# Kernel optimization log

Measured on AMD Instinct MI355X. Metric: run time of the kernel, lower is better.

## Reference

```python
import jax, jax.numpy as jnp
import numpy as np

# Tree: 64 leaves (16 feat -> 16 out), 8 mids (16 feat + 8*16 child = 144 -> 32 out),
# root (16 feat + 8*32 child = 272 -> 64 out), head -> 10 tasks. Eval-mode BatchNorm.
B = 16384
EPS = 1e-5


def setup_inputs() -> dict:
    key = jax.random.key(0)
    ks = jax.random.split(key, 24)
    rn = lambda k, s: jax.random.normal(k, s, dtype=jnp.float32)
    ru = lambda k, s: jax.random.uniform(k, s, dtype=jnp.float32)
    return {
        "x": rn(ks[0], (B, 1168)),
        # leaf layers (64 nodes, 16 -> 16)
        "Wl": rn(ks[1], (64, 16, 16)) * 0.1, "bl": rn(ks[2], (64, 16)) * 0.1,
        "gl": ru(ks[3], (64, 16)) + 0.5, "betal": rn(ks[4], (64, 16)) * 0.1,
        "ml": rn(ks[5], (64, 16)) * 0.1, "vl": ru(ks[6], (64, 16)) + 0.5,
        # mid layers (8 nodes, 144 -> 32)
        "Wm": rn(ks[7], (8, 144, 32)) * 0.1, "bm": rn(ks[8], (8, 32)) * 0.1,
        "gm": ru(ks[9], (8, 32)) + 0.5, "betam": rn(ks[10], (8, 32)) * 0.1,
        "mm": rn(ks[11], (8, 32)) * 0.1, "vm": ru(ks[12], (8, 32)) + 0.5,
        # root layer (272 -> 64)
        "Wr": rn(ks[13], (272, 64)) * 0.1, "br": rn(ks[14], (64,)) * 0.1,
        "gr": ru(ks[15], (64,)) + 0.5, "betar": rn(ks[16], (64,)) * 0.1,
        "mr": rn(ks[17], (64,)) * 0.1, "vr": ru(ks[18], (64,)) + 0.5,
        # root prediction head (64 -> 10 tasks)
        "Wh": rn(ks[19], (64, 10)) * 0.1, "bh": rn(ks[20], (10,)) * 0.1,
    }


def _bn(h, g, b, m, v):
    return (h - m) * jax.lax.rsqrt(v + EPS) * g + b


def reference(x, Wl, bl, gl, betal, ml, vl, Wm, bm, gm, betam, mm, vm,
              Wr, br, gr, betar, mr, vr, Wh, bh):
    n = x.shape[0]
    # leaves: gather own features (contiguous layout), Linear+BN+Tanh, batched over 64 nodes
    xl = x[:, :1024].reshape(n, 64, 16)
    hl = jnp.tanh(_bn(jnp.einsum('bli,lio->blo', xl, Wl) + bl, gl, betal, ml, vl))
    # mids: concat own features with 8 leaf-child outputs -> [n, 8, 144]
    xm = x[:, 1024:1152].reshape(n, 8, 16)
    mid_in = jnp.concatenate([xm, hl.reshape(n, 8, 128)], axis=-1)
    hm = jnp.tanh(_bn(jnp.einsum('bmi,mio->bmo', mid_in, Wm) + bm, gm, betam, mm, vm))
    # root: concat own features with 8 mid outputs -> [n, 272]
    root_in = jnp.concatenate([x[:, 1152:1168], hm.reshape(n, 256)], axis=-1)
    hr = jnp.tanh(_bn(root_in @ Wr + br, gr, betar, mr, vr))
    # root prediction head (eval-mode forward returns only root prediction)
    return hr @ Wh + bh
```

## Files before the change

kernel.cpp:

```cpp
#include <hip/hip_runtime.h>

typedef __attribute__((ext_vector_type(8))) short bf16x8;
typedef __attribute__((ext_vector_type(4))) float f32x4;

#define EPS 1e-5f

#define N_FRAG_BLOCKS 182
#define WSB_LEAF 0
#define WSB_MID  64
#define WSB_ROOT 144
#define WSB_HEAD 180
#define ST_SL 0
#define ST_TL 1024
#define ST_SM 2048
#define ST_TM 2304
#define ST_SR 2560
#define ST_TR 2624
#define WS_ST_BYTE_OFF (N_FRAG_BLOCKS * 1024)

__device__ __forceinline__ unsigned short f2bf(float f) {
    unsigned u = __float_as_uint(f);
    unsigned r = u + 0x7fffu + ((u >> 16) & 1u);
    return (unsigned short)(r >> 16);
}

__device__ __forceinline__ unsigned pack2bf(float a, float b) {
    return (unsigned)f2bf(a) | ((unsigned)f2bf(b) << 16);
}

__device__ __forceinline__ bf16x8 pack8(float4 a, float4 b) {
    union { unsigned u[4]; bf16x8 v; } r;
    r.u[0] = pack2bf(a.x, a.y); r.u[1] = pack2bf(a.z, a.w);
    r.u[2] = pack2bf(b.x, b.y); r.u[3] = pack2bf(b.z, b.w);
    return r.v;
}

__device__ __forceinline__ float tanh_fast(float x) {
    float e = __expf(2.0f * x);
    return 1.0f - 2.0f / (e + 1.0f);
}

__global__ void ontology_prep(
    const float* __restrict__ Wl, const float* __restrict__ Wm,
    const float* __restrict__ Wr, const float* __restrict__ Wh,
    const float* __restrict__ bl, const float* __restrict__ gl,
    const float* __restrict__ betal, const float* __restrict__ ml,
    const float* __restrict__ vl,
    const float* __restrict__ bm, const float* __restrict__ gm,
    const float* __restrict__ betam, const float* __restrict__ mm,
    const float* __restrict__ vm,
    const float* __restrict__ br, const float* __restrict__ gr,
    const float* __restrict__ betar, const float* __restrict__ mr,
    const float* __restrict__ vr,
    unsigned short* __restrict__ wsFrag, float* __restrict__ wsST)
{
    const int b = blockIdx.x;
    const int t = threadIdx.x;
    if (b < N_FRAG_BLOCKS) {
        const int row = t & 15, g = t >> 4;
        unsigned short vals[8];
        #pragma unroll
        for (int i = 0; i < 8; ++i) {
            const int k = g * 8 + i;
            float v = 0.f;
            if (b < 64) {
                const int l = b;
                if ((l & 1) == 0) { if (k < 16)  v = Wl[l * 256 + k * 16 + row]; }
                else              { if (k >= 16) v = Wl[l * 256 + (k - 16) * 16 + row]; }
            } else if (b < 144) {
                const int idx = b - 64, m = idx / 10, rem = idx % 10;
                const int tt = rem / 5, s = rem % 5;
                const int krow = s * 32 + k;
                if (krow < 144) v = Wm[m * 4608 + krow * 32 + tt * 16 + row];
            } else if (b < 180) {
                const int idx = b - 144, tt = idx / 9, s = idx % 9;
                if (s == 0) { if (k < 16) v = Wr[k * 64 + tt * 16 + row]; }
                else { const int krow = 16 + (s - 1) * 32 + k;
                       v = Wr[krow * 64 + tt * 16 + row]; }
            } else {
                const int s = b - 180, krow = s * 32 + k;
                if (row < 10) v = Wh[krow * 10 + row];
            }
            vals[i] = f2bf(v);
        }
        #pragma unroll
        for (int i = 0; i < 8; ++i) wsFrag[b * 512 + t * 8 + i] = vals[i];
    } else if (b == N_FRAG_BLOCKS) {
        for (int i = 0; i < 16; ++i) {
            const int id = t + 64 * i;
            const float S = gl[id] * rsqrtf(vl[id] + EPS);
            wsST[ST_SL + id] = S;
            wsST[ST_TL + id] = (bl[id] - ml[id]) * S + betal[id];
        }
    } else if (b == N_FRAG_BLOCKS + 1) {
        for (int i = 0; i < 4; ++i) {
            const int id = t + 64 * i;
            const float S = gm[id] * rsqrtf(vm[id] + EPS);
            wsST[ST_SM + id] = S;
            wsST[ST_TM + id] = (bm[id] - mm[id]) * S + betam[id];
        }
    } else {
        const int id = t;
        const float S = gr[id] * rsqrtf(vr[id] + EPS);
        wsST[ST_SR + id] = S;
        wsST[ST_TR + id] = (br[id] - mr[id]) * S + betar[id];
    }
}

__global__ __launch_bounds__(256, 4) void ontology_mfma(
    const float* __restrict__ x,
    const unsigned short* __restrict__ wsFrag,
    const float* __restrict__ wsST,
    const float* __restrict__ bh,
    float* __restrict__ out)
{
    __shared__ __align__(16) unsigned short mid_in[4][16][168];
    __shared__ __align__(16) unsigned short hm[16][264];
    unsigned short (*hr)[72] = (unsigned short (*)[72])&mid_in[0][0][0];

    const int w    = threadIdx.x >> 6;
    const int lane = threadIdx.x & 63;
    const int c    = lane & 15;
    const int g    = lane >> 4;
    const int rowbase = blockIdx.x * 16;
    const float* xrow = x + (size_t)(rowbase + c) * 1168;

    {
        uint2 z = {0u, 0u};
        *(uint2*)&mid_in[w][c][144 + 4 * g] = z;
    }

    const float* Sl = wsST + ST_SL, *Tl = wsST + ST_TL;
    const float* Sm = wsST + ST_SM, *Tm = wsST + ST_TM;
    const float* Sr = wsST + ST_SR, *Tr = wsST + ST_TR;

    #pragma unroll 1
    for (int mi = 0; mi < 2; ++mi) {
        const int mm = w * 2 + mi;
        {
            float4 xm4 = *(const float4*)(xrow + 1024 + mm * 16 + 4 * g);
            uint2 p; p.x = pack2bf(xm4.x, xm4.y); p.y = pack2bf(xm4.z, xm4.w);
            *(uint2*)&mid_in[w][c][4 * g] = p;
        }
        #pragma unroll
        for (int p = 0; p < 4; ++p) {
            const int pair = mm * 4 + p;
            const float* xp = xrow + pair * 32 + g * 8;
            float4 xa = *(const float4*)xp;
            float4 xb = *(const float4*)(xp + 4);
            bf16x8 bfrag = pack8(xa, xb);
            #pragma unroll
            for (int e = 0; e < 2; ++e) {
                const int leaf = pair * 2 + e;
                bf16x8 afrag = *(const bf16x8*)(wsFrag + (WSB_LEAF + leaf) * 512 + lane * 8);
                f32x4 acc = {0.f, 0.f, 0.f, 0.f};
                acc = __builtin_amdgcn_mfma_f32_16x16x32_bf16(afrag, bfrag, acc, 0, 0, 0);
                float4 S = *(const float4*)(Sl + leaf * 16 + 4 * g);
                float4 T = *(const float4*)(Tl + leaf * 16 + 4 * g);
                float h0 = tanh_fast(acc[0] * S.x + T.x);
                float h1 = tanh_fast(acc[1] * S.y + T.y);
                float h2 = tanh_fast(acc[2] * S.z + T.z);
                float h3 = tanh_fast(acc[3] * S.w + T.w);
                uint2 pk; pk.x = pack2bf(h0, h1); pk.y = pack2bf(h2, h3);
                *(uint2*)&mid_in[w][c][16 + (p * 2 + e) * 16 + 4 * g] = pk;
            }
        }
        {
            f32x4 acc0 = {0.f, 0.f, 0.f, 0.f};
            f32x4 acc1 = {0.f, 0.f, 0.f, 0.f};
            const unsigned short* fb = wsFrag + (WSB_MID + mm * 10) * 512 + lane * 8;
            #pragma unroll
            for (int s = 0; s < 5; ++s) {
                bf16x8 bfrag = *(const bf16x8*)&mid_in[w][c][s * 32 + g * 8];
                bf16x8 a0 = *(const bf16x8*)(fb + s * 512);
                bf16x8 a1 = *(const bf16x8*)(fb + (5 + s) * 512);
                acc0 = __builtin_amdgcn_mfma_f32_16x16x32_bf16(a0, bfrag, acc0, 0, 0, 0);
                acc1 = __builtin_amdgcn_mfma_f32_16x16x32_bf16(a1, bfrag, acc1, 0, 0, 0);
            }
            #pragma unroll
            for (int t = 0; t < 2; ++t) {
                f32x4 acc = t ? acc1 : acc0;
                const int po = mm * 32 + t * 16 + 4 * g;
                float4 S = *(const float4*)(Sm + po);
                float4 T = *(const float4*)(Tm + po);
                float h0 = tanh_fast(acc[0] * S.x + T.x);
                float h1 = tanh_fast(acc[1] * S.y + T.y);
                float h2 = tanh_fast(acc[2] * S.z + T.z);
                float h3 = tanh_fast(acc[3] * S.w + T.w);
                uint2 pk; pk.x = pack2bf(h0, h1); pk.y = pack2bf(h2, h3);
                *(uint2*)&hm[c][po] = pk;
            }
        }
    }
    __syncthreads();

    {
        f32x4 acc = {0.f, 0.f, 0.f, 0.f};
        const unsigned short* fb = wsFrag + (WSB_ROOT + w * 9) * 512 + lane * 8;
        {
            const float* xp = xrow + 1152 + (g & 1) * 8;
            float4 xa = *(const float4*)xp;
            float4 xb = *(const float4*)(xp + 4);
            bf16x8 bfrag = pack8(xa, xb);
            bf16x8 a0 = *(const bf16x8*)fb;
            acc = __builtin_amdgcn_mfma_f32_16x16x32_bf16(a0, bfrag, acc, 0, 0, 0);
        }
        #pragma unroll
        for (int s = 1; s <= 8; ++s) {
            bf16x8 bfrag = *(const bf16x8*)&hm[c][(s - 1) * 32 + g * 8];
            bf16x8 a0 = *(const bf16x8*)(fb + s * 512);
            acc = __builtin_amdgcn_mfma_f32_16x16x32_bf16(a0, bfrag, acc, 0, 0, 0);
        }
        const int po = w * 16 + 4 * g;
        float4 S = *(const float4*)(Sr + po);
        float4 T = *(const float4*)(Tr + po);
        float h0 = tanh_fast(acc[0] * S.x + T.x);
        float h1 = tanh_fast(acc[1] * S.y + T.y);
        float h2 = tanh_fast(acc[2] * S.z + T.z);
        float h3 = tanh_fast(acc[3] * S.w + T.w);
        uint2 pk; pk.x = pack2bf(h0, h1); pk.y = pack2bf(h2, h3);
        *(uint2*)&hr[c][po] = pk;
    }
    __syncthreads();

    if (w == 0) {
        f32x4 acc = {0.f, 0.f, 0.f, 0.f};
        #pragma unroll
        for (int s = 0; s < 2; ++s) {
            bf16x8 bfrag = *(const bf16x8*)&hr[c][s * 32 + g * 8];
            bf16x8 a0 = *(const bf16x8*)(wsFrag + (WSB_HEAD + s) * 512 + lane * 8);
            acc = __builtin_amdgcn_mfma_f32_16x16x32_bf16(a0, bfrag, acc, 0, 0, 0);
        }
        float* op = out + (size_t)(rowbase + c) * 10 + 4 * g;
        if (g < 2) {
            float2 o1 = {acc[0] + bh[4 * g],     acc[1] + bh[4 * g + 1]};
            float2 o2 = {acc[2] + bh[4 * g + 2], acc[3] + bh[4 * g + 3]};
            *(float2*)op = o1;
            *(float2*)(op + 2) = o2;
        } else if (g == 2) {
            float2 o1 = {acc[0] + bh[8], acc[1] + bh[9]};
            *(float2*)op = o1;
        }
    }
}

extern "C" void kernel_launch(void* const* d_in, const int* in_sizes, int n_in,
                              void* d_out, int out_size, void* d_ws, size_t ws_size,
                              hipStream_t stream) {
    const float* x     = (const float*)d_in[0];
    const float* Wl    = (const float*)d_in[1];
    const float* bl    = (const float*)d_in[2];
    const float* gl    = (const float*)d_in[3];
    const float* betal = (const float*)d_in[4];
    const float* ml    = (const float*)d_in[5];
    const float* vl    = (const float*)d_in[6];
    const float* Wm    = (const float*)d_in[7];
    const float* bm    = (const float*)d_in[8];
    const float* gm    = (const float*)d_in[9];
    const float* betam = (const float*)d_in[10];
    const float* mm    = (const float*)d_in[11];
    const float* vm    = (const float*)d_in[12];
    const float* Wr    = (const float*)d_in[13];
    const float* br    = (const float*)d_in[14];
    const float* gr    = (const float*)d_in[15];
    const float* betar = (const float*)d_in[16];
    const float* mr    = (const float*)d_in[17];
    const float* vr    = (const float*)d_in[18];
    const float* Wh    = (const float*)d_in[19];
    const float* bh    = (const float*)d_in[20];
    float* out = (float*)d_out;

    unsigned short* wsFrag = (unsigned short*)d_ws;
    float* wsST = (float*)((char*)d_ws + WS_ST_BYTE_OFF);

    ontology_prep<<<N_FRAG_BLOCKS + 3, 64, 0, stream>>>(
        Wl, Wm, Wr, Wh, bl, gl, betal, ml, vl, bm, gm, betam, mm, vm,
        br, gr, betar, mr, vr, wsFrag, wsST);

    const int n = in_sizes[0] / 1168;
    ontology_mfma<<<n / 16, 256, 0, stream>>>(x, wsFrag, wsST, bh, out);
}
```

Measured before the change: 35.55 us.

## Use single-wave blocks with triple-buffered async global-to-LDS staging of x

Replaces the 4-wave block with a single 64-thread wave that processes all 8 mid subtrees in sequence for 16 rows. Input features for each mid are prefetched into a three-slot LDS ring with global_load_lds, and explicit vmcnt waits overlap the loads with MFMA work. The root accumulation is folded incrementally into the mid loop, which removes the __syncthreads barriers. The trade-off is less parallelism per block and heavier LDS use (~33KB per block), which may limit occupancy. Correctness also depends on the hand-counted vmcnt values.

New measurement: 58.99 us. 1.66x slower.

```diff
diff --git a/kernel.cpp b/kernel.cpp
--- a/kernel.cpp
+++ b/kernel.cpp
@@ -107,54 +107,96 @@
     }
 }
 
-__global__ __launch_bounds__(256, 4) void ontology_mfma(
+__global__ __launch_bounds__(64, 2) void ontology_mfma(
     const float* __restrict__ x,
     const unsigned short* __restrict__ wsFrag,
     const float* __restrict__ wsST,
     const float* __restrict__ bh,
     float* __restrict__ out)
 {
-    __shared__ __align__(16) unsigned short mid_in[4][16][168];
-    __shared__ __align__(16) unsigned short hm[16][264];
-    unsigned short (*hr)[72] = (unsigned short (*)[72])&mid_in[0][0][0];
-
-    const int w    = threadIdx.x >> 6;
-    const int lane = threadIdx.x & 63;
-    const int c    = lane & 15;
-    const int g    = lane >> 4;
+    __shared__ __align__(16) float xs[3][2560];
+    __shared__ __align__(16) unsigned short mid_in[16][168];
+    __shared__ __align__(16) unsigned short hm[16][40];
+    __shared__ __align__(16) unsigned short hr[16][72];
+
+    const int lane = threadIdx.x;
+    const int c = lane & 15;
+    const int g = lane >> 4;
     const int rowbase = blockIdx.x * 16;
     const float* xrow = x + (size_t)(rowbase + c) * 1168;
 
+    const float* Sl = wsST + ST_SL; const float* Tl = wsST + ST_TL;
+    const float* Sm = wsST + ST_SM; const float* Tm = wsST + ST_TM;
+    const float* Sr = wsST + ST_SR; const float* Tr = wsST + ST_TR;
+
+    auto stage = [&](int mid, int b) {
+        float* dst = &xs[b][0];
+        #pragma unroll
+        for (int k = 0; k < 10; ++k) {
+            const int fo = k * 256 + lane * 4;
+            const int row = fo / 148;
+            const int col = fo - row * 148;
+            const float* src;
+            if ((row < 16) & (col < 144)) {
+                const float* xr = x + (size_t)(rowbase + row) * 1168;
+                src = (col < 16) ? (xr + 1024 + mid * 16 + col)
+                                 : (xr + (mid * 128 - 16) + col);
+            } else {
+                src = xrow;
+            }
+            __builtin_amdgcn_global_load_lds(
+                (const __attribute__((address_space(1))) unsigned int*)src,
+                (__attribute__((address_space(3))) unsigned int*)(dst + k * 256),
+                16, 0, 0);
+        }
+    };
+
+    stage(0, 0);
+    stage(1, 1);
+
     {
-        uint2 z = {0u, 0u};
-        *(uint2*)&mid_in[w][c][144 + 4 * g] = z;
-    }
-
-    const float* Sl = wsST + ST_SL, *Tl = wsST + ST_TL;
-    const float* Sm = wsST + ST_SM, *Tm = wsST + ST_TM;
-    const float* Sr = wsST + ST_SR, *Tr = wsST + ST_TR;
+        uint2 z; z.x = 0u; z.y = 0u;
+        *(uint2*)&mid_in[c][144 + 4 * g] = z;
+    }
+
+    f32x4 accR[4];
+    {
+        const float* xp = xrow + 1152 + (g & 1) * 8;
+        float4 xa = *(const float4*)xp;
+        float4 xb = *(const float4*)(xp + 4);
+        bf16x8 bfrag = pack8(xa, xb);
+        #pragma unroll
+        for (int t = 0; t < 4; ++t) {
+            bf16x8 a = *(const bf16x8*)(wsFrag + (WSB_ROOT + t * 9) * 512 + lane * 8);
+            f32x4 zz = {0.f, 0.f, 0.f, 0.f};
+            accR[t] = __builtin_amdgcn_mfma_f32_16x16x32_bf16(a, bfrag, zz, 0, 0, 0);
+        }
+    }
 
     #pragma unroll 1
-    for (int mi = 0; mi < 2; ++mi) {
-        const int mm = w * 2 + mi;
+    for (int mi = 0; mi < 8; ++mi) {
+        const int b = mi % 3;
+        if (mi < 7) { asm volatile("s_waitcnt vmcnt(10)" ::: "memory"); }
+        else        { asm volatile("s_waitcnt vmcnt(0)" ::: "memory"); }
+        const float* xb_ = &xs[b][0];
+
         {
-            float4 xm4 = *(const float4*)(xrow + 1024 + mm * 16 + 4 * g);
-            uint2 p; p.x = pack2bf(xm4.x, xm4.y); p.y = pack2bf(xm4.z, xm4.w);
-            *(uint2*)&mid_in[w][c][4 * g] = p;
+            float4 xm4 = *(const float4*)(xb_ + c * 148 + 4 * g);
+            uint2 pm; pm.x = pack2bf(xm4.x, xm4.y); pm.y = pack2bf(xm4.z, xm4.w);
+            *(uint2*)&mid_in[c][4 * g] = pm;
         }
         #pragma unroll
         for (int p = 0; p < 4; ++p) {
-            const int pair = mm * 4 + p;
-            const float* xp = xrow + pair * 32 + g * 8;
+            const float* xp = xb_ + c * 148 + 16 + p * 32 + g * 8;
             float4 xa = *(const float4*)xp;
-            float4 xb = *(const float4*)(xp + 4);
-            bf16x8 bfrag = pack8(xa, xb);
+            float4 x2 = *(const float4*)(xp + 4);
+            bf16x8 bfrag = pack8(xa, x2);
             #pragma unroll
             for (int e = 0; e < 2; ++e) {
-                const int leaf = pair * 2 + e;
+                const int leaf = mi * 8 + p * 2 + e;
                 bf16x8 afrag = *(const bf16x8*)(wsFrag + (WSB_LEAF + leaf) * 512 + lane * 8);
-                f32x4 acc = {0.f, 0.f, 0.f, 0.f};
-                acc = __builtin_amdgcn_mfma_f32_16x16x32_bf16(afrag, bfrag, acc, 0, 0, 0);
+                f32x4 zz = {0.f, 0.f, 0.f, 0.f};
+                f32x4 acc = __builtin_amdgcn_mfma_f32_16x16x32_bf16(afrag, bfrag, zz, 0, 0, 0);
                 float4 S = *(const float4*)(Sl + leaf * 16 + 4 * g);
                 float4 T = *(const float4*)(Tl + leaf * 16 + 4 * g);
                 float h0 = tanh_fast(acc[0] * S.x + T.x);
@@ -162,16 +204,16 @@
                 float h2 = tanh_fast(acc[2] * S.z + T.z);
                 float h3 = tanh_fast(acc[3] * S.w + T.w);
                 uint2 pk; pk.x = pack2bf(h0, h1); pk.y = pack2bf(h2, h3);
-                *(uint2*)&mid_in[w][c][16 + (p * 2 + e) * 16 + 4 * g] = pk;
+                *(uint2*)&mid_in[c][16 + (p * 2 + e) * 16 + 4 * g] = pk;
             }
         }
         {
             f32x4 acc0 = {0.f, 0.f, 0.f, 0.f};
             f32x4 acc1 = {0.f, 0.f, 0.f, 0.f};
-            const unsigned short* fb = wsFrag + (WSB_MID + mm * 10) * 512 + lane * 8;
+            const unsigned short* fb = wsFrag + (WSB_MID + mi * 10) * 512 + lane * 8;
             #pragma unroll
             for (int s = 0; s < 5; ++s) {
-                bf16x8 bfrag = *(const bf16x8*)&mid_in[w][c][s * 32 + g * 8];
+                bf16x8 bfrag = *(const bf16x8*)&mid_in[c][s * 32 + g * 8];
                 bf16x8 a0 = *(const bf16x8*)(fb + s * 512);
                 bf16x8 a1 = *(const bf16x8*)(fb + (5 + s) * 512);
                 acc0 = __builtin_amdgcn_mfma_f32_16x16x32_bf16(a0, bfrag, acc0, 0, 0, 0);
@@ -180,7 +222,7 @@
             #pragma unroll
             for (int t = 0; t < 2; ++t) {
                 f32x4 acc = t ? acc1 : acc0;
-                const int po = mm * 32 + t * 16 + 4 * g;
+                const int po = mi * 32 + t * 16 + 4 * g;
                 float4 S = *(const float4*)(Sm + po);
                 float4 T = *(const float4*)(Tm + po);
                 float h0 = tanh_fast(acc[0] * S.x + T.x);
@@ -188,48 +230,40 @@
                 float h2 = tanh_fast(acc[2] * S.z + T.z);
                 float h3 = tanh_fast(acc[3] * S.w + T.w);
                 uint2 pk; pk.x = pack2bf(h0, h1); pk.y = pack2bf(h2, h3);
-                *(uint2*)&hm[c][po] = pk;
-            }
-        }
-    }
-    __syncthreads();
+                *(uint2*)&hm[c][t * 16 + 4 * g] = pk;
+            }
+        }
+        {
+            bf16x8 bfrag = *(const bf16x8*)&hm[c][g * 8];
+            #pragma unroll
+            for (int t = 0; t < 4; ++t) {
+                bf16x8 a = *(const bf16x8*)(wsFrag + (WSB_ROOT + t * 9 + mi + 1) * 512 + lane * 8);
+                accR[t] = __builtin_amdgcn_mfma_f32_16x16x32_bf16(a, bfrag, accR[t], 0, 0, 0);
+            }
+        }
+        if (mi < 6) stage(mi + 2, (mi + 2) % 3);
+    }
+
+    #pragma unroll
+    for (int t = 0; t < 4; ++t) {
+        const int po = t * 16 + 4 * g;
+        float4 S = *(const float4*)(Sr + po);
+        float4 T = *(const float4*)(Tr + po);
+        float h0 = tanh_fast(accR[t][0] * S.x + T.x);
+        float h1 = tanh_fast(accR[t][1] * S.y + T.y);
+        float h2 = tanh_fast(accR[t][2] * S.z + T.z);
+        float h3 = tanh_fast(accR[t][3] * S.w + T.w);
+        uint2 pk; pk.x = pack2bf(h0, h1); pk.y = pack2bf(h2, h3);
+        *(uint2*)&hr[c][po] = pk;
+    }
 
     {
         f32x4 acc = {0.f, 0.f, 0.f, 0.f};
-        const unsigned short* fb = wsFrag + (WSB_ROOT + w * 9) * 512 + lane * 8;
-        {
-            const float* xp = xrow + 1152 + (g & 1) * 8;
-            float4 xa = *(const float4*)xp;
-            float4 xb = *(const float4*)(xp + 4);
-            bf16x8 bfrag = pack8(xa, xb);
-            bf16x8 a0 = *(const bf16x8*)fb;
-            acc = __builtin_amdgcn_mfma_f32_16x16x32_bf16(a0, bfrag, acc, 0, 0, 0);
-        }
-        #pragma unroll
-        for (int s = 1; s <= 8; ++s) {
-            bf16x8 bfrag = *(const bf16x8*)&hm[c][(s - 1) * 32 + g * 8];
-            bf16x8 a0 = *(const bf16x8*)(fb + s * 512);
-            acc = __builtin_amdgcn_mfma_f32_16x16x32_bf16(a0, bfrag, acc, 0, 0, 0);
-        }
-        const int po = w * 16 + 4 * g;
-        float4 S = *(const float4*)(Sr + po);
-        float4 T = *(const float4*)(Tr + po);
-        float h0 = tanh_fast(acc[0] * S.x + T.x);
-        float h1 = tanh_fast(acc[1] * S.y + T.y);
-        float h2 = tanh_fast(acc[2] * S.z + T.z);
-        float h3 = tanh_fast(acc[3] * S.w + T.w);
-        uint2 pk; pk.x = pack2bf(h0, h1); pk.y = pack2bf(h2, h3);
-        *(uint2*)&hr[c][po] = pk;
-    }
-    __syncthreads();
-
-    if (w == 0) {
-        f32x4 acc = {0.f, 0.f, 0.f, 0.f};
         #pragma unroll
         for (int s = 0; s < 2; ++s) {
             bf16x8 bfrag = *(const bf16x8*)&hr[c][s * 32 + g * 8];
-            bf16x8 a0 = *(const bf16x8*)(wsFrag + (WSB_HEAD + s) * 512 + lane * 8);
-            acc = __builtin_amdgcn_mfma_f32_16x16x32_bf16(a0, bfrag, acc, 0, 0, 0);
+            bf16x8 a = *(const bf16x8*)(wsFrag + (WSB_HEAD + s) * 512 + lane * 8);
+            acc = __builtin_amdgcn_mfma_f32_16x16x32_bf16(a, bfrag, acc, 0, 0, 0);
         }
         float* op = out + (size_t)(rowbase + c) * 10 + 4 * g;
         if (g < 2) {
@@ -278,5 +312,5 @@
         br, gr, betar, mr, vr, wsFrag, wsST);
 
     const int n = in_sizes[0] / 1168;
-    ontology_mfma<<<n / 16, 256, 0, stream>>>(x, wsFrag, wsST, bh, out);
-}
+    ontology_mfma<<<n / 16, 64, 0, stream>>>(x, wsFrag, wsST, bh, out);
+}
```

## Use eight waves per block, one mid node each, and fold tanh scaling into BN

Applied to the files above, without the earlier changes.

Blocks grow from four waves to eight, so each wave handles one mid node and its eight leaves instead of looping over two mids. All x loads for a wave are issued up front to expose more memory-level parallelism. The mid outputs are written into each wave's own LDS region and read by the root stage. The BN scale and shift are prescaled by 2/ln2 in the prep kernel so the activation becomes exp2 plus a hardware reciprocal, with no division. Only half the waves take part in the root stage, and the larger blocks raise register and LDS pressure per block.

After: 31.93 us. 1.11x faster.

```diff
diff --git a/kernel.cpp b/kernel.cpp
--- a/kernel.cpp
+++ b/kernel.cpp
@@ -4,6 +4,7 @@
 typedef __attribute__((ext_vector_type(4))) float f32x4;
 
 #define EPS 1e-5f
+#define K2L 2.8853900817779268f
 
 #define N_FRAG_BLOCKS 182
 #define WSB_LEAF 0
@@ -35,9 +36,10 @@
     return r.v;
 }
 
-__device__ __forceinline__ float tanh_fast(float x) {
-    float e = __expf(2.0f * x);
-    return 1.0f - 2.0f / (e + 1.0f);
+__device__ __forceinline__ float bn_act(float acc, float Sp, float Tp) {
+    float e = exp2f(fmaf(acc, Sp, Tp));
+    float r = __builtin_amdgcn_rcpf(e + 1.0f);
+    return fmaf(-2.0f, r, 1.0f);
 }
 
 __global__ void ontology_prep(
@@ -89,145 +91,146 @@
         for (int i = 0; i < 16; ++i) {
             const int id = t + 64 * i;
             const float S = gl[id] * rsqrtf(vl[id] + EPS);
-            wsST[ST_SL + id] = S;
-            wsST[ST_TL + id] = (bl[id] - ml[id]) * S + betal[id];
+            wsST[ST_SL + id] = S * K2L;
+            wsST[ST_TL + id] = ((bl[id] - ml[id]) * S + betal[id]) * K2L;
         }
     } else if (b == N_FRAG_BLOCKS + 1) {
         for (int i = 0; i < 4; ++i) {
             const int id = t + 64 * i;
             const float S = gm[id] * rsqrtf(vm[id] + EPS);
-            wsST[ST_SM + id] = S;
-            wsST[ST_TM + id] = (bm[id] - mm[id]) * S + betam[id];
+            wsST[ST_SM + id] = S * K2L;
+            wsST[ST_TM + id] = ((bm[id] - mm[id]) * S + betam[id]) * K2L;
         }
     } else {
         const int id = t;
         const float S = gr[id] * rsqrtf(vr[id] + EPS);
-        wsST[ST_SR + id] = S;
-        wsST[ST_TR + id] = (br[id] - mr[id]) * S + betar[id];
-    }
-}
-
-__global__ __launch_bounds__(256, 4) void ontology_mfma(
+        wsST[ST_SR + id] = S * K2L;
+        wsST[ST_TR + id] = ((br[id] - mr[id]) * S + betar[id]) * K2L;
+    }
+}
+
+__global__ __launch_bounds__(512, 8) void ontology_mfma(
     const float* __restrict__ x,
     const unsigned short* __restrict__ wsFrag,
     const float* __restrict__ wsST,
     const float* __restrict__ bh,
     float* __restrict__ out)
 {
-    __shared__ __align__(16) unsigned short mid_in[4][16][168];
-    __shared__ __align__(16) unsigned short hm[16][264];
-    unsigned short (*hr)[72] = (unsigned short (*)[72])&mid_in[0][0][0];
-
-    const int w    = threadIdx.x >> 6;
-    const int lane = threadIdx.x & 63;
+    __shared__ __align__(16) unsigned short lds[8 * 2560];
+
+    const int tid  = threadIdx.x;
+    const int w    = tid >> 6;
+    const int lane = tid & 63;
     const int c    = lane & 15;
     const int g    = lane >> 4;
     const int rowbase = blockIdx.x * 16;
     const float* xrow = x + (size_t)(rowbase + c) * 1168;
 
+    unsigned short* my = lds + w * 2560;
+    unsigned short* hr = lds + 7 * 2560 + 1280;
+
+    const float* Sl = wsST + ST_SL; const float* Tl = wsST + ST_TL;
+    const float* Sm = wsST + ST_SM; const float* Tm = wsST + ST_TM;
+    const float* Sr = wsST + ST_SR; const float* Tr = wsST + ST_TR;
+
+    { uint2 z; z.x = 0u; z.y = 0u;
+      *(uint2*)(my + c * 160 + 144 + 4 * g) = z; }
+
+    float4 xm4 = *(const float4*)(xrow + 1024 + w * 16 + 4 * g);
+    float4 xp[4][2];
+    #pragma unroll
+    for (int p = 0; p < 4; ++p) {
+        const float* a = xrow + (w * 4 + p) * 32 + g * 8;
+        xp[p][0] = *(const float4*)a;
+        xp[p][1] = *(const float4*)(a + 4);
+    }
+
+    { uint2 pm; pm.x = pack2bf(xm4.x, xm4.y); pm.y = pack2bf(xm4.z, xm4.w);
+      *(uint2*)(my + c * 160 + 4 * g) = pm; }
+
+    #pragma unroll
+    for (int p = 0; p < 4; ++p) {
+        bf16x8 bfrag = pack8(xp[p][0], xp[p][1]);
+        #pragma unroll
+        for (int e = 0; e < 2; ++e) {
+            const int l = 2 * p + e, leaf = w * 8 + l;
+            bf16x8 afrag = *(const bf16x8*)(wsFrag + (WSB_LEAF + leaf) * 512 + lane * 8);
+            f32x4 zz = {0.f,0.f,0.f,0.f};
+            f32x4 acc = __builtin_amdgcn_mfma_f32_16x16x32_bf16(afrag, bfrag, zz, 0, 0, 0);
+            const int po = leaf * 16 + 4 * g;
+            float4 S = *(const float4*)(Sl + po);
+            float4 T = *(const float4*)(Tl + po);
+            uint2 pk;
+            pk.x = pack2bf(bn_act(acc[0], S.x, T.x), bn_act(acc[1], S.y, T.y));
+            pk.y = pack2bf(bn_act(acc[2], S.z, T.z), bn_act(acc[3], S.w, T.w));
+            *(uint2*)(my + c * 160 + 16 + l * 16 + 4 * g) = pk;
+        }
+    }
+
     {
-        uint2 z = {0u, 0u};
-        *(uint2*)&mid_in[w][c][144 + 4 * g] = z;
-    }
-
-    const float* Sl = wsST + ST_SL, *Tl = wsST + ST_TL;
-    const float* Sm = wsST + ST_SM, *Tm = wsST + ST_TM;
-    const float* Sr = wsST + ST_SR, *Tr = wsST + ST_TR;
-
-    #pragma unroll 1
-    for (int mi = 0; mi < 2; ++mi) {
-        const int mm = w * 2 + mi;
+        f32x4 acc0 = {0.f,0.f,0.f,0.f};
+        f32x4 acc1 = {0.f,0.f,0.f,0.f};
+        const unsigned short* fb = wsFrag + (WSB_MID + w * 10) * 512 + lane * 8;
+        #pragma unroll
+        for (int s = 0; s < 5; ++s) {
+            bf16x8 bfrag = *(const bf16x8*)(my + c * 160 + s * 32 + g * 8);
+            bf16x8 a0 = *(const bf16x8*)(fb + s * 512);
+            bf16x8 a1 = *(const bf16x8*)(fb + (5 + s) * 512);
+            acc0 = __builtin_amdgcn_mfma_f32_16x16x32_bf16(a0, bfrag, acc0, 0, 0, 0);
+            acc1 = __builtin_amdgcn_mfma_f32_16x16x32_bf16(a1, bfrag, acc1, 0, 0, 0);
+        }
+        #pragma unroll
+        for (int tt = 0; tt < 2; ++tt) {
+            f32x4 acc = tt ? acc1 : acc0;
+            const int po = w * 32 + tt * 16 + 4 * g;
+            float4 S = *(const float4*)(Sm + po);
+            float4 T = *(const float4*)(Tm + po);
+            uint2 pk;
+            pk.x = pack2bf(bn_act(acc[0], S.x, T.x), bn_act(acc[1], S.y, T.y));
+            pk.y = pack2bf(bn_act(acc[2], S.z, T.z), bn_act(acc[3], S.w, T.w));
+            *(uint2*)(my + c * 40 + tt * 16 + 4 * g) = pk;
+        }
+    }
+
+    float4 xrA, xrB;
+    if (w < 4) {
+        const float* rp = xrow + 1152 + (g & 1) * 8;
+        xrA = *(const float4*)rp;
+        xrB = *(const float4*)(rp + 4);
+    }
+
+    __syncthreads();
+
+    if (w < 4) {
+        const unsigned short* fb = wsFrag + (WSB_ROOT + w * 9) * 512 + lane * 8;
+        f32x4 acc = {0.f,0.f,0.f,0.f};
         {
-            float4 xm4 = *(const float4*)(xrow + 1024 + mm * 16 + 4 * g);
-            uint2 p; p.x = pack2bf(xm4.x, xm4.y); p.y = pack2bf(xm4.z, xm4.w);
-            *(uint2*)&mid_in[w][c][4 * g] = p;
-        }
-        #pragma unroll
-        for (int p = 0; p < 4; ++p) {
-            const int pair = mm * 4 + p;
-            const float* xp = xrow + pair * 32 + g * 8;
-            float4 xa = *(const float4*)xp;
-            float4 xb = *(const float4*)(xp + 4);
-            bf16x8 bfrag = pack8(xa, xb);
-            #pragma unroll
-            for (int e = 0; e < 2; ++e) {
-                const int leaf = pair * 2 + e;
-                bf16x8 afrag = *(const bf16x8*)(wsFrag + (WSB_LEAF + leaf) * 512 + lane * 8);
-                f32x4 acc = {0.f, 0.f, 0.f, 0.f};
-                acc = __builtin_amdgcn_mfma_f32_16x16x32_bf16(afrag, bfrag, acc, 0, 0, 0);
-                float4 S = *(const float4*)(Sl + leaf * 16 + 4 * g);
-                float4 T = *(const float4*)(Tl + leaf * 16 + 4 * g);
-                float h0 = tanh_fast(acc[0] * S.x + T.x);
-                float h1 = tanh_fast(acc[1] * S.y + T.y);
-                float h2 = tanh_fast(acc[2] * S.z + T.z);
-                float h3 = tanh_fast(acc[3] * S.w + T.w);
-                uint2 pk; pk.x = pack2bf(h0, h1); pk.y = pack2bf(h2, h3);
-                *(uint2*)&mid_in[w][c][16 + (p * 2 + e) * 16 + 4 * g] = pk;
-            }
-        }
-        {
-            f32x4 acc0 = {0.f, 0.f, 0.f, 0.f};
-            f32x4 acc1 = {0.f, 0.f, 0.f, 0.f};
-            const unsigned short* fb = wsFrag + (WSB_MID + mm * 10) * 512 + lane * 8;
-            #pragma unroll
-            for (int s = 0; s < 5; ++s) {
-                bf16x8 bfrag = *(const bf16x8*)&mid_in[w][c][s * 32 + g * 8];
-                bf16x8 a0 = *(const bf16x8*)(fb + s * 512);
-                bf16x8 a1 = *(const bf16x8*)(fb + (5 + s) * 512);
-                acc0 = __builtin_amdgcn_mfma_f32_16x16x32_bf16(a0, bfrag, acc0, 0, 0, 0);
-                acc1 = __builtin_amdgcn_mfma_f32_16x16x32_bf16(a1, bfrag, acc1, 0, 0, 0);
-            }
-            #pragma unroll
-            for (int t = 0; t < 2; ++t) {
-                f32x4 acc = t ? acc1 : acc0;
-                const int po = mm * 32 + t * 16 + 4 * g;
-                float4 S = *(const float4*)(Sm + po);
-                float4 T = *(const float4*)(Tm + po);
-                float h0 = tanh_fast(acc[0] * S.x + T.x);
-                float h1 = tanh_fast(acc[1] * S.y + T.y);
-                float h2 = tanh_fast(acc[2] * S.z + T.z);
-                float h3 = tanh_fast(acc[3] * S.w + T.w);
-                uint2 pk; pk.x = pack2bf(h0, h1); pk.y = pack2bf(h2, h3);
-                *(uint2*)&hm[c][po] = pk;
-            }
-        }
-    }
-    __syncthreads();
-
-    {
-        f32x4 acc = {0.f, 0.f, 0.f, 0.f};
-        const unsigned short* fb = wsFrag + (WSB_ROOT + w * 9) * 512 + lane * 8;
-        {
-            const float* xp = xrow + 1152 + (g & 1) * 8;
-            float4 xa = *(const float4*)xp;
-            float4 xb = *(const float4*)(xp + 4);
-            bf16x8 bfrag = pack8(xa, xb);
+            bf16x8 bfrag = pack8(xrA, xrB);
             bf16x8 a0 = *(const bf16x8*)fb;
             acc = __builtin_amdgcn_mfma_f32_16x16x32_bf16(a0, bfrag, acc, 0, 0, 0);
         }
         #pragma unroll
         for (int s = 1; s <= 8; ++s) {
-            bf16x8 bfrag = *(const bf16x8*)&hm[c][(s - 1) * 32 + g * 8];
+            bf16x8 bfrag = *(const bf16x8*)(lds + (s - 1) * 2560 + c * 40 + g * 8);
             bf16x8 a0 = *(const bf16x8*)(fb + s * 512);
             acc = __builtin_amdgcn_mfma_f32_16x16x32_bf16(a0, bfrag, acc, 0, 0, 0);
         }
         const int po = w * 16 + 4 * g;
         float4 S = *(const float4*)(Sr + po);
         float4 T = *(const float4*)(Tr + po);
-        float h0 = tanh_fast(acc[0] * S.x + T.x);
-        float h1 = tanh_fast(acc[1] * S.y + T.y);
-        float h2 = tanh_fast(acc[2] * S.z + T.z);
-        float h3 = tanh_fast(acc[3] * S.w + T.w);
-        uint2 pk; pk.x = pack2bf(h0, h1); pk.y = pack2bf(h2, h3);
-        *(uint2*)&hr[c][po] = pk;
-    }
+        uint2 pk;
+        pk.x = pack2bf(bn_act(acc[0], S.x, T.x), bn_act(acc[1], S.y, T.y));
+        pk.y = pack2bf(bn_act(acc[2], S.z, T.z), bn_act(acc[3], S.w, T.w));
+        *(uint2*)(hr + c * 72 + w * 16 + 4 * g) = pk;
+    }
+
     __syncthreads();
 
     if (w == 0) {
-        f32x4 acc = {0.f, 0.f, 0.f, 0.f};
+        f32x4 acc = {0.f,0.f,0.f,0.f};
         #pragma unroll
         for (int s = 0; s < 2; ++s) {
-            bf16x8 bfrag = *(const bf16x8*)&hr[c][s * 32 + g * 8];
+            bf16x8 bfrag = *(const bf16x8*)(hr + c * 72 + s * 32 + g * 8);
             bf16x8 a0 = *(const bf16x8*)(wsFrag + (WSB_HEAD + s) * 512 + lane * 8);
             acc = __builtin_amdgcn_mfma_f32_16x16x32_bf16(a0, bfrag, acc, 0, 0, 0);
         }
@@ -278,5 +281,5 @@
         br, gr, betar, mr, vr, wsFrag, wsST);
 
     const int n = in_sizes[0] / 1168;
-    ontology_mfma<<<n / 16, 256, 0, stream>>>(x, wsFrag, wsST, bh, out);
-}
+    ontology_mfma<<<n / 16, 512, 0, stream>>>(x, wsFrag, wsST, bh, out);
+}
```
